# Performance work log

Measured on AMD Instinct MI355X. Metric: run time of the kernel, lower is better.

## Reference

```python
import jax, jax.numpy as jnp
import numpy as np

B, C, H, W = 16, 3, 128, 128
PATCH = 8
E = 512          # embedding_dim
NH = 8           # num_heads
P = 64           # proj_dim
HID = 2048       # hidden_dim
L = 6            # num_layers
COND = 3
PH, PW = H // PATCH, W // PATCH
S = PH * PW + 1  # sequence length (patches + cond token)
INV_SQRT_E = 1.0 / np.float32(np.sqrt(E))

_PARAM_SHAPES = {
    'patch_w': (E, C, PATCH, PATCH), 'patch_b': (E,),
    'cond_w1': (COND, E), 'cond_b1': (E,), 'cond_w2': (E, E), 'cond_b2': (E,),
    'pos_embed': (1, S, E),
    'enc_vp': (L, NH, E, P), 'enc_kp': (L, NH, E, P), 'enc_qh': (L, NH, S, S), 'enc_lift': (L, 1, NH * P, E),
    'enc_ln1g': (L, E), 'enc_ln1b': (L, E),
    'enc_w1': (L, E, HID), 'enc_b1': (L, HID), 'enc_w2': (L, HID, E), 'enc_b2': (L, E),
    'enc_ln2g': (L, E), 'enc_ln2b': (L, E),
    'dec_vp': (L, NH, E, P), 'dec_kp': (L, NH, E, P), 'dec_qh': (L, NH, S, S), 'dec_lift': (L, 1, NH * P, E),
    'dec_ln2g': (L, E), 'dec_ln2b': (L, E),
    'dec_w1': (L, E, HID), 'dec_b1': (L, HID), 'dec_w2': (L, HID, E), 'dec_b2': (L, E),
    'dec_ln3g': (L, E), 'dec_ln3b': (L, E),
    'final_g': (E,), 'final_b': (E,),
    'deconv_w': (E, C, PATCH, PATCH), 'deconv_b': (C,),
}


def setup_inputs() -> dict:
    key = jax.random.key(0)
    inp = {
        'x': jax.random.normal(jax.random.fold_in(key, 1000), (B, C, H, W), jnp.float32),
        'y': jax.random.normal(jax.random.fold_in(key, 1001), (B, COND), jnp.float32),
    }
    for i, (name, shp) in enumerate(_PARAM_SHAPES.items()):
        w = 0.02 * jax.random.normal(jax.random.fold_in(key, i), shp, jnp.float32)
        if name.endswith('g'):  # layernorm gains near 1
            w = w + 1.0
        inp[name] = w
    return inp


def _ln(x, g, b, eps=1e-5):
    m = x.mean(-1, keepdims=True)
    v = ((x - m) ** 2).mean(-1, keepdims=True)
    return (x - m) * jax.lax.rsqrt(v + eps) * g + b


def _mhsa(x, vp, kp, qh, lift):
    # x: (B,S,E); vp/kp: (NH,E,P); qh: (NH,S,S); lift: (1, NH*P, E)
    k = jnp.einsum('bse,hep->bhsp', x, kp)
    v = jnp.einsum('bse,hep->bhsp', x, vp)
    qv = jnp.einsum('hst,bhtp->bhsp', qh, v)
    # a_ts = (qh@V) @ K^T, then transpose(-2,-1): a[t,s] = qv[s] . k[t]
    a = jnp.einsum('bhsp,bhtp->bhts', qv, k) * INV_SQRT_E
    a = jax.nn.softmax(a, axis=-1)
    o = jnp.einsum('bhst,bhtp->bhsp', a, v)          # (B,NH,S,P)
    o = o.transpose(0, 2, 1, 3).reshape(x.shape[0], S, NH * P)
    return o @ lift[0]


def _block(z, vp, kp, qh, lift, g1, b1, w1, fb1, w2, fb2, g2, b2):
    z = _ln(z + _mhsa(z, vp, kp, qh, lift), g1, b1)
    h = jax.nn.leaky_relu(z @ w1 + fb1, 0.2) @ w2 + fb2  # dropout = identity (eval)
    return _ln(z + h, g2, b2)


def reference(x, y, patch_w, patch_b, cond_w1, cond_b1, cond_w2, cond_b2, pos_embed,
              enc_vp, enc_kp, enc_qh, enc_lift, enc_ln1g, enc_ln1b,
              enc_w1, enc_b1, enc_w2, enc_b2, enc_ln2g, enc_ln2b,
              dec_vp, dec_kp, dec_qh, dec_lift, dec_ln2g, dec_ln2b,
              dec_w1, dec_b1, dec_w2, dec_b2, dec_ln3g, dec_ln3b,
              final_g, final_b, deconv_w, deconv_b):
    b = x.shape[0]
    # Patching: Conv2d(k=p, s=p) == block-reshape + einsum
    xp = x.reshape(b, C, PH, PATCH, PW, PATCH)
    tok = jnp.einsum('bchpwq,ecpq->bhwe', xp, patch_w).reshape(b, PH * PW, E) + patch_b
    cond = jax.nn.leaky_relu(y @ cond_w1 + cond_b1, 0.2)
    cond = jax.nn.leaky_relu(cond @ cond_w2 + cond_b2, 0.2)
    z = jnp.concatenate([cond[:, None, :], tok], axis=1) + pos_embed
    for i in range(L):
        z = _block(z, enc_vp[i], enc_kp[i], enc_qh[i], enc_lift[i],
                   enc_ln1g[i], enc_ln1b[i], enc_w1[i], enc_b1[i],
                   enc_w2[i], enc_b2[i], enc_ln2g[i], enc_ln2b[i])
    for i in range(L):  # decoder: only mhsa_2 / ln2 / ff / ln3 are used
        z = _block(z, dec_vp[i], dec_kp[i], dec_qh[i], dec_lift[i],
                   dec_ln2g[i], dec_ln2b[i], dec_w1[i], dec_b1[i],
                   dec_w2[i], dec_b2[i], dec_ln3g[i], dec_ln3b[i])
    z = _ln(z[:, 1:], final_g, final_b)               # drop cond token
    g = z.reshape(b, PH, PW, E)                        # (B,E,PH,PW) grid, channels-last form
    out = jnp.einsum('bhwe,ecpq->bchpwq', g, deconv_w).reshape(b, C, H, W)
    return out + deconv_b[None, :, None, None]
```

## Files before the change

kernel.cpp:

```cpp
#include <hip/hip_runtime.h>
#include <stdint.h>
#include <math.h>

#define B_    16
#define C_    3
#define HIMG  128
#define E_    512
#define NH_   8
#define S_    257
#define T_    256
#define MTOK  4096
#define MSEQ  4112
#define HID_  2048
#define SP_   288
#define SLAB  (288*288)
#define PS    2105344L
#define INV_SQRT_E 0.044194173824159216f

typedef __attribute__((ext_vector_type(8))) __bf16 bf16x8;
typedef __attribute__((ext_vector_type(4))) float f32x4;

__device__ __forceinline__ void gload16(const void* g, const void* lds)
{
    __builtin_amdgcn_global_load_lds(
        (const __attribute__((address_space(1))) uint32_t*)(uintptr_t)g,
        (__attribute__((address_space(3))) uint32_t*)(uint32_t)(uintptr_t)lds,
        16, 0, 0);
}

template<int WMW, int WNW, bool LEAKY, bool OUTF32, bool VSPLIT>
__device__ __forceinline__ void gemm_core(
    const __bf16* __restrict__ A, int lda,
    const __bf16* __restrict__ Bt, int ldb,
    void* __restrict__ C, int ldc,
    const float* __restrict__ bias, float scale,
    int M, int N, int K, int tm, int tn, __bf16* __restrict__ vTout)
{
    constexpr int BM  = WMW * 64;
    constexpr int BN  = WNW * 32;
    constexpr int T   = WMW * WNW * 64;
    constexpr int ACH = BM * 4;
    constexpr int BCH = BN * 4;
    constexpr int LPT = ACH / T + BCH / T;
    __shared__ __align__(16) __bf16 sA[4][BM * 32];
    __shared__ __align__(16) __bf16 sB[4][BN * 32];

    const int tid  = threadIdx.x;
    const int lane = tid & 63;
    const int wid  = tid >> 6;
    const int wm   = wid / WNW;
    const int wn   = wid % WNW;
    const int lh   = lane >> 4;
    const int ll   = lane & 15;

    const __bf16* Ab = A + (long)tm * BM * lda;
    const __bf16* Bb = Bt + (long)tn * BN * ldb;

    f32x4 acc[4][2] = {};
    const int nst = K >> 5;

    auto stage = [&](int buf, int k0) {
#pragma unroll
        for (int rr = 0; rr < ACH / T; ++rr) {
            const int L = rr * T + tid;
            const int row = L >> 2;
            const int gch = (L & 3) ^ ((row >> 1) & 3);
            gload16(Ab + (long)row * lda + k0 + gch * 8,
                    (const char*)(&sA[buf][0]) + (rr * T + (wid << 6)) * 16);
        }
#pragma unroll
        for (int rr = 0; rr < BCH / T; ++rr) {
            const int L = rr * T + tid;
            const int row = L >> 2;
            const int gch = (L & 3) ^ ((row >> 1) & 3);
            gload16(Bb + (long)row * ldb + k0 + gch * 8,
                    (const char*)(&sB[buf][0]) + (rr * T + (wid << 6)) * 16);
        }
    };

    const int PF = nst < 3 ? nst : 3;
    for (int s = 0; s < PF; ++s) stage(s & 3, s << 5);

    for (int st = 0; st < nst; ++st) {
        const int rem = nst - 1 - st;
        if (rem >= 2)      asm volatile("s_waitcnt vmcnt(%0)" :: "n"(2 * LPT) : "memory");
        else if (rem == 1) asm volatile("s_waitcnt vmcnt(%0)" :: "n"(LPT) : "memory");
        else               asm volatile("s_waitcnt vmcnt(0)" ::: "memory");
        __builtin_amdgcn_s_barrier();
        __builtin_amdgcn_sched_barrier(0);

        if (st + 3 < nst) stage((st + 3) & 3, (st + 3) << 5);

        const int cur = st & 3;
        bf16x8 afr[4], bfr[2];
#pragma unroll
        for (int i = 0; i < 4; ++i) {
            const int rw = wm * 64 + i * 16 + ll;
            const int c  = lh ^ ((rw >> 1) & 3);
            afr[i] = *reinterpret_cast<const bf16x8*>(&sA[cur][rw * 32 + c * 8]);
        }
#pragma unroll
        for (int j = 0; j < 2; ++j) {
            const int rw = wn * 32 + j * 16 + ll;
            const int c  = lh ^ ((rw >> 1) & 3);
            bfr[j] = *reinterpret_cast<const bf16x8*>(&sB[cur][rw * 32 + c * 8]);
        }
#pragma unroll
        for (int i = 0; i < 4; ++i)
#pragma unroll
            for (int j = 0; j < 2; ++j)
                acc[i][j] = __builtin_amdgcn_mfma_f32_16x16x32_bf16(
                                afr[i], bfr[j], acc[i][j], 0, 0, 0);
    }

#pragma unroll
    for (int i = 0; i < 4; ++i)
#pragma unroll
        for (int ii = 0; ii < 4; ++ii) {
            const int m = tm * BM + wm * 64 + i * 16 + lh * 4 + ii;
            if (m >= M) continue;
#pragma unroll
            for (int j = 0; j < 2; ++j) {
                const int n = tn * BN + wn * 32 + j * 16 + ll;
                if (n >= N) continue;
                float v = acc[i][j][ii] * scale;
                if (bias) v += bias[n];
                if (LEAKY) v = v > 0.f ? v : 0.2f * v;
                if (VSPLIT && n >= 512) {
                    const int b = m / S_;
                    const int t = m - b * S_;
                    const int hp = n - 512;
                    vTout[(((long)(b * 8 + (hp >> 6)) * 64) + (hp & 63)) * SP_ + t] =
                        (__bf16)v;
                } else if (OUTF32) {
                    ((float*)C)[(long)m * ldc + n] = v;
                } else {
                    ((__bf16*)C)[(long)m * ldc + n] = (__bf16)v;
                }
            }
        }
}

__device__ __forceinline__ int xcd_swizzle(int wg, int nwg)
{
    const int q = nwg >> 3, r = nwg & 7;
    if (q == 0) return wg;
    const int xcd = wg & 7, off = wg >> 3;
    return (xcd < r ? xcd * (q + 1) : r * (q + 1) + (xcd - r) * q) + off;
}

template<int WMW, int WNW, bool LEAKY, bool OUTF32, bool VSPLIT>
__global__ __launch_bounds__(WMW * WNW * 64) void gemm_k(
    const __bf16* __restrict__ A, int lda, const __bf16* __restrict__ Bt, int ldb,
    void* __restrict__ C, int ldc, const float* __restrict__ bias, float scale,
    int M, int N, int K, int ntn, __bf16* __restrict__ vTout)
{
    const int wg = xcd_swizzle(blockIdx.x, gridDim.x);
    gemm_core<WMW, WNW, LEAKY, OUTF32, VSPLIT>(A, lda, Bt, ldb, C, ldc, bias, scale,
                                               M, N, K, wg / ntn, wg % ntn, vTout);
}

template<int WMW, int WNW>
__global__ __launch_bounds__(WMW * WNW * 64) void gemm_split_k(
    const __bf16* __restrict__ A, int lda, const __bf16* __restrict__ Bt, int ldb,
    __bf16* __restrict__ P, long pstride, const float* __restrict__ bias,
    int M, int N, int K, int npart, int ntn)
{
    const int part = blockIdx.y;
    const int Kp = K / npart;
    const int wg = xcd_swizzle(blockIdx.x, gridDim.x);
    gemm_core<WMW, WNW, false, false, false>(A + (long)part * Kp, lda,
                                             Bt + (long)part * Kp, ldb,
                                             P + (long)part * pstride, N,
                                             part == 0 ? bias : nullptr, 1.f,
                                             M, N, Kp, wg / ntn, wg % ntn, nullptr);
}

__global__ __launch_bounds__(256) void qv_k(const __bf16* __restrict__ qhb,
                                            const __bf16* __restrict__ vT,
                                            __bf16* __restrict__ qvcat)
{
    const int bh = blockIdx.z, b = bh >> 3, h = bh & 7;
    gemm_core<2, 2, false, false, false>(qhb + (long)h * SLAB, SP_,
                                         vT + (long)bh * 64 * SP_, SP_,
                                         qvcat + (long)b * S_ * E_ + h * 64, E_,
                                         nullptr, 1.f, S_, 64, SP_, blockIdx.x, 0,
                                         nullptr);
}

__global__ __launch_bounds__(256) void fa_k(const __bf16* __restrict__ kcat,
                                            const __bf16* __restrict__ qvcat,
                                            const __bf16* __restrict__ vT,
                                            __bf16* __restrict__ ocat)
{
    __shared__ __align__(16) __bf16 sK[64 * 64], sQV[64 * 64], sV[64 * 64];
    __shared__ __align__(16) __bf16 sP[4][16 * 64];
    const int bh = blockIdx.y, b = bh >> 3, h = bh & 7;
    const int i0 = blockIdx.x * 64;
    const int tid = threadIdx.x, lane = tid & 63, wid = tid >> 6;
    const int ll = lane & 15, lh = lane >> 4;

    const __bf16* kSrc = kcat + ((long)(b * S_ + i0)) * 512 + h * 64;
    const __bf16* qvB  = qvcat + (long)b * S_ * E_ + h * 64;
    const __bf16* vTb  = vT + (long)bh * 64 * SP_;

    auto stage64 = [&](__bf16* lds, const __bf16* src, int ldsrc) {
#pragma unroll
        for (int r = 0; r < 2; ++r) {
            const int L = r * 256 + wid * 64 + lane;
            const int row = L >> 3, c = L & 7;
            const int sc = c ^ (row & 7);
            gload16(src + (long)row * ldsrc + sc * 8,
                    (const char*)lds + (r * 256 + wid * 64) * 16);
        }
    };

    stage64(sK, kSrc, 512);
    stage64(sQV, qvB, E_);
    stage64(sV, vTb, SP_);
    __syncthreads();

    bf16x8 ka[2];
#pragma unroll
    for (int ks = 0; ks < 2; ++ks) {
        const int row = wid * 16 + ll;
        ka[ks] = *reinterpret_cast<const bf16x8*>(
            &sK[row * 64 + (((ks * 4 + lh) ^ (row & 7)) << 3)]);
    }

    float m[4], l[4];
#pragma unroll
    for (int ii = 0; ii < 4; ++ii) { m[ii] = -1e30f; l[ii] = 0.f; }
    f32x4 oacc[4] = {};

    for (int jt = 0; jt < 5; ++jt) {
        const int j0 = jt * 64;
        f32x4 s[4] = {};
#pragma unroll
        for (int ks = 0; ks < 2; ++ks)
#pragma unroll
            for (int nf = 0; nf < 4; ++nf) {
                const int row = nf * 16 + ll;
                const bf16x8 qb = *reinterpret_cast<const bf16x8*>(
                    &sQV[row * 64 + (((ks * 4 + lh) ^ (row & 7)) << 3)]);
                s[nf] = __builtin_amdgcn_mfma_f32_16x16x32_bf16(ka[ks], qb, s[nf], 0, 0, 0);
            }
        float pv[4][4];
#pragma unroll
        for (int ii = 0; ii < 4; ++ii) {
            float mx = -1e30f;
#pragma unroll
            for (int nf = 0; nf < 4; ++nf) {
                float sv = s[nf][ii] * INV_SQRT_E;
                if (j0 + nf * 16 + ll >= S_) sv = -1e30f;
                pv[nf][ii] = sv;
                mx = fmaxf(mx, sv);
            }
#pragma unroll
            for (int msk = 1; msk < 16; msk <<= 1) mx = fmaxf(mx, __shfl_xor(mx, msk));
            const float mnew = fmaxf(m[ii], mx);
            const float resc = __expf(m[ii] - mnew);
            m[ii] = mnew;
            float sum = 0.f;
#pragma unroll
            for (int nf = 0; nf < 4; ++nf) {
                const float e = __expf(pv[nf][ii] - mnew);
                pv[nf][ii] = e; sum += e;
            }
#pragma unroll
            for (int msk = 1; msk < 16; msk <<= 1) sum += __shfl_xor(sum, msk);
            l[ii] = l[ii] * resc + sum;
#pragma unroll
            for (int pf = 0; pf < 4; ++pf) oacc[pf][ii] *= resc;
        }
        __bf16* sPw = &sP[wid][0];
#pragma unroll
        for (int nf = 0; nf < 4; ++nf)
#pragma unroll
            for (int ii = 0; ii < 4; ++ii) {
                const int row = lh * 4 + ii, col = ll + 16 * nf;
                sPw[row * 64 + ((((col >> 3) ^ (row & 7)) << 3) | (col & 7))] =
                    (__bf16)pv[nf][ii];
            }
#pragma unroll
        for (int ks = 0; ks < 2; ++ks) {
            const bf16x8 pa = *reinterpret_cast<const bf16x8*>(
                &sPw[ll * 64 + (((ks * 4 + lh) ^ (ll & 7)) << 3)]);
#pragma unroll
            for (int pf = 0; pf < 4; ++pf) {
                const int row = pf * 16 + ll;
                const bf16x8 vb = *reinterpret_cast<const bf16x8*>(
                    &sV[row * 64 + (((ks * 4 + lh) ^ (row & 7)) << 3)]);
                oacc[pf] = __builtin_amdgcn_mfma_f32_16x16x32_bf16(pa, vb, oacc[pf], 0, 0, 0);
            }
        }
        if (jt < 4) {
            __syncthreads();
            stage64(sQV, qvB + (long)(j0 + 64) * E_, E_);
            stage64(sV, vTb + j0 + 64, SP_);
            __syncthreads();
        }
    }
#pragma unroll
    for (int ii = 0; ii < 4; ++ii) {
        const int i = i0 + wid * 16 + lh * 4 + ii;
        if (i >= S_) continue;
        const float invl = 1.f / l[ii];
#pragma unroll
        for (int pf = 0; pf < 4; ++pf)
            ocat[((long)(b * S_ + i)) * E_ + h * 64 + pf * 16 + ll] =
                (__bf16)(oacc[pf][ii] * invl);
    }
}

__global__ void ln_kernel(const __bf16* x,
                          const __bf16* __restrict__ parts, int nparts, long pstride,
                          const float* __restrict__ g, const float* __restrict__ bb,
                          __bf16* outb, int skip_cond, int nrows)
{
    const int row = blockIdx.x * 4 + (threadIdx.x >> 6);
    if (row >= nrows) return;
    const int lane = threadIdx.x & 63;
    const long xrow = skip_cond ? (long)row + (row >> 8) + 1 : (long)row;
    const bf16x8 xa = *reinterpret_cast<const bf16x8*>(x + xrow * E_ + lane * 8);
    float e[8];
#pragma unroll
    for (int i = 0; i < 8; ++i) e[i] = (float)xa[i];
    for (int p = 0; p < nparts; ++p) {
        const bf16x8 pv = *reinterpret_cast<const bf16x8*>(
            parts + (long)p * pstride + (long)row * E_ + lane * 8);
#pragma unroll
        for (int i = 0; i < 8; ++i) e[i] += (float)pv[i];
    }
    float s = 0.f;
#pragma unroll
    for (int i = 0; i < 8; ++i) s += e[i];
#pragma unroll
    for (int o = 32; o; o >>= 1) s += __shfl_xor(s, o);
    const float mean = s * (1.f / 512.f);
    float v = 0.f;
#pragma unroll
    for (int i = 0; i < 8; ++i) { e[i] -= mean; v += e[i] * e[i]; }
#pragma unroll
    for (int o = 32; o; o >>= 1) v += __shfl_xor(v, o);
    const float inv = rsqrtf(v * (1.f / 512.f) + 1e-5f);
    const float4* gp = (const float4*)g + lane * 2;
    const float4* bp = (const float4*)bb + lane * 2;
    const float4 g0 = gp[0], g1 = gp[1], bb0 = bp[0], bb1 = bp[1];
    const float gv[8] = {g0.x, g0.y, g0.z, g0.w, g1.x, g1.y, g1.z, g1.w};
    const float bv[8] = {bb0.x, bb0.y, bb0.z, bb0.w, bb1.x, bb1.y, bb1.z, bb1.w};
    bf16x8 ov;
#pragma unroll
    for (int i = 0; i < 8; ++i) ov[i] = (__bf16)(e[i] * inv * gv[i] + bv[i]);
    *reinterpret_cast<bf16x8*>(outb + (long)row * E_ + lane * 8) = ov;
}

__global__ void conv_straight(const float* __restrict__ in, __bf16* __restrict__ out, long n)
{
    const long i = (long)blockIdx.x * 256 + threadIdx.x;
    if (i < n) out[i] = (__bf16)in[i];
}

__global__ void conv_transpose(const float* __restrict__ in, __bf16* __restrict__ out,
                               int R, int C)
{
    __shared__ float tile[32][33];
    const int r0 = blockIdx.x * 32, c0 = blockIdx.y * 32;
    const int tx = threadIdx.x & 31, ty = threadIdx.x >> 5;
#pragma unroll
    for (int i = 0; i < 32; i += 8) {
        const int rr = r0 + ty + i, cc = c0 + tx;
        tile[ty + i][tx] = (rr < R && cc < C) ? in[(long)rr * C + cc] : 0.f;
    }
    __syncthreads();
#pragma unroll
    for (int i = 0; i < 32; i += 8) {
        const int cc = c0 + ty + i, rr = r0 + tx;
        if (cc < C && rr < R) out[(long)cc * R + rr] = (__bf16)tile[tx][ty + i];
    }
}

__global__ void wconv_all(const float* __restrict__ enc_kp, const float* __restrict__ dec_kp,
                          const float* __restrict__ enc_vp, const float* __restrict__ dec_vp,
                          const float* __restrict__ enc_lift, const float* __restrict__ dec_lift,
                          const float* __restrict__ enc_w1, const float* __restrict__ dec_w1,
                          const float* __restrict__ enc_w2, const float* __restrict__ dec_w2,
                          __bf16* __restrict__ kvT, __bf16* __restrict__ liftT,
                          __bf16* __restrict__ w1T, __bf16* __restrict__ w2T)
{
    const int lyr = blockIdx.z;
    const bool enc = lyr < 6;
    const int li = enc ? lyr : lyr - 6;
    const int j = blockIdx.y;
    const float* src; __bf16* dst; int R, C, nb;
    switch (j) {
        case 0:  src = (enc ? enc_kp : dec_kp) + (long)li * 262144;
                 dst = kvT + (long)lyr * 524288;            R = 512; C = 64;   nb = 8; break;
        case 1:  src = (enc ? enc_vp : dec_vp) + (long)li * 262144;
                 dst = kvT + (long)lyr * 524288 + 262144;   R = 512; C = 64;   nb = 8; break;
        case 2:  src = (enc ? enc_lift : dec_lift) + (long)li * 262144;
                 dst = liftT + (long)lyr * 262144;          R = 512; C = 512;  nb = 1; break;
        case 3:  src = (enc ? enc_w1 : dec_w1) + (long)li * 1048576;
                 dst = w1T + (long)lyr * 1048576;           R = 512; C = 2048; nb = 1; break;
        default: src = (enc ? enc_w2 : dec_w2) + (long)li * 1048576;
                 dst = w2T + (long)lyr * 1048576;           R = 2048; C = 512; nb = 1; break;
    }
    const int tR = R >> 5, tC = C >> 5;
    int t = blockIdx.x;
    if (t >= tR * tC * nb) return;
    const int bt = t / (tR * tC);
    t %= tR * tC;
    const int rt = t / tC, ct = t % tC;
    const long bs = (long)R * C;
    const float* ip = src + (long)bt * bs;
    __bf16* op = dst + (long)bt * bs;
    __shared__ float tile[32][33];
    const int tx = threadIdx.x & 31, ty = threadIdx.x >> 5;
#pragma unroll
    for (int i = 0; i < 32; i += 8)
        tile[ty + i][tx] = ip[(long)(rt * 32 + ty + i) * C + ct * 32 + tx];
    __syncthreads();
#pragma unroll
    for (int i = 0; i < 32; i += 8)
        op[(long)(ct * 32 + ty + i) * R + rt * 32 + tx] = (__bf16)tile[tx][ty + i];
}

__global__ void conv_qh_all(const float* __restrict__ enc_qh,
                            const float* __restrict__ dec_qh,
                            __bf16* __restrict__ out)
{
    const long n = 12L * 8 * SLAB;
    for (long o = (long)blockIdx.x * 256 + threadIdx.x; o < n; o += (long)gridDim.x * 256) {
        const int t = (int)(o % SP_);
        const long rr = o / SP_;
        const int s = (int)(rr % SP_);
        const long hh = rr / SP_;
        const int h = (int)(hh % 8);
        const int lyr = (int)(hh / 8);
        float v = 0.f;
        if (s < S_ && t < S_) {
            const float* src = (lyr < 6 ? enc_qh + (long)lyr * 8 * S_ * S_
                                        : dec_qh + (long)(lyr - 6) * 8 * S_ * S_);
            v = src[((long)h * S_ + s) * S_ + t];
        }
        out[o] = (__bf16)v;
    }
}

__global__ void vpad_kernel(__bf16* __restrict__ vT)
{
    const int i = blockIdx.x * 256 + threadIdx.x;
    if (i >= 128 * 64 * 31) return;
    const int t = 257 + (i % 31);
    const long rp = i / 31;
    vT[rp * SP_ + t] = (__bf16)0.f;
}

__global__ void im2col_kernel(const float* __restrict__ x, __bf16* __restrict__ xcol)
{
    const int idx = blockIdx.x * 256 + threadIdx.x;
    if (idx >= MTOK * 192) return;
    const int m = idx / 192, k = idx % 192;
    const int b = m >> 8, t = m & 255;
    const int ph = t >> 4, pw = t & 15;
    const int c = k >> 6, rr = k & 63;
    const int p = rr >> 3, q = rr & 7;
    xcol[idx] = (__bf16)x[(((long)(b * C_ + c) * HIMG) + ph * 8 + p) * HIMG + pw * 8 + q];
}

__global__ void cond_kernel(const float* __restrict__ y,
                            const float* __restrict__ w1, const float* __restrict__ b1,
                            const float* __restrict__ w2, const float* __restrict__ b2,
                            const float* __restrict__ pos, __bf16* __restrict__ zb)
{
    __shared__ float c1[512];
    const int b = blockIdx.x;
    const int e = threadIdx.x;
    float v = y[b * 3 + 0] * w1[e] + y[b * 3 + 1] * w1[512 + e]
            + y[b * 3 + 2] * w1[1024 + e] + b1[e];
    v = v > 0.f ? v : 0.2f * v;
    c1[e] = v;
    __syncthreads();
    float acc = b2[e];
    for (int k = 0; k < 512; ++k) acc += c1[k] * w2[k * 512 + e];
    acc = acc > 0.f ? acc : 0.2f * acc;
    zb[(long)b * S_ * E_ + e] = (__bf16)(acc + pos[e]);
}

__global__ void assemble_kernel(const __bf16* __restrict__ tok,
                                const float* __restrict__ pos,
                                __bf16* __restrict__ zb)
{
    const int idx = blockIdx.x * 256 + threadIdx.x;
    if (idx >= MTOK * E_) return;
    const int m = idx >> 9;
    const int e = idx & 511;
    const int b = m >> 8, t = m & 255;
    const float o = (float)tok[idx] + pos[(1 + t) * E_ + e];
    zb[((long)b * S_ + 1 + t) * E_ + e] = (__bf16)o;
}

__global__ void scatter_kernel(const float* __restrict__ dtmp,
                               const float* __restrict__ db,
                               float* __restrict__ out)
{
    const int idx = blockIdx.x * 256 + threadIdx.x;
    if (idx >= B_ * C_ * HIMG * HIMG) return;
    const int b  = idx / (C_ * HIMG * HIMG);
    const int rm = idx % (C_ * HIMG * HIMG);
    const int c  = rm / (HIMG * HIMG);
    const int hh = (rm % (HIMG * HIMG)) / HIMG;
    const int ww = rm % HIMG;
    const int ph = hh >> 3, p = hh & 7;
    const int pw = ww >> 3, q = ww & 7;
    out[idx] = dtmp[((long)(b * 256 + ph * 16 + pw)) * 192 + c * 64 + p * 8 + q] + db[c];
}

extern "C" void kernel_launch(void* const* d_in, const int* in_sizes, int n_in,
                              void* d_out, int out_size, void* d_ws, size_t ws_size,
                              hipStream_t stream)
{
    const float* x        = (const float*)d_in[0];
    const float* y        = (const float*)d_in[1];
    const float* patch_w  = (const float*)d_in[2];
    const float* patch_b  = (const float*)d_in[3];
    const float* cond_w1  = (const float*)d_in[4];
    const float* cond_b1  = (const float*)d_in[5];
    const float* cond_w2  = (const float*)d_in[6];
    const float* cond_b2  = (const float*)d_in[7];
    const float* pos      = (const float*)d_in[8];
    const float* enc_vp   = (const float*)d_in[9];
    const float* enc_kp   = (const float*)d_in[10];
    const float* enc_qh   = (const float*)d_in[11];
    const float* enc_lift = (const float*)d_in[12];
    const float* enc_ln1g = (const float*)d_in[13];
    const float* enc_ln1b = (const float*)d_in[14];
    const float* enc_w1   = (const float*)d_in[15];
    const float* enc_b1   = (const float*)d_in[16];
    const float* enc_w2   = (const float*)d_in[17];
    const float* enc_b2   = (const float*)d_in[18];
    const float* enc_ln2g = (const float*)d_in[19];
    const float* enc_ln2b = (const float*)d_in[20];
    const float* dec_vp   = (const float*)d_in[21];
    const float* dec_kp   = (const float*)d_in[22];
    const float* dec_qh   = (const float*)d_in[23];
    const float* dec_lift = (const float*)d_in[24];
    const float* dec_ln2g = (const float*)d_in[25];
    const float* dec_ln2b = (const float*)d_in[26];
    const float* dec_w1   = (const float*)d_in[27];
    const float* dec_b1   = (const float*)d_in[28];
    const float* dec_w2   = (const float*)d_in[29];
    const float* dec_b2   = (const float*)d_in[30];
    const float* dec_ln3g = (const float*)d_in[31];
    const float* dec_ln3b = (const float*)d_in[32];
    const float* final_g  = (const float*)d_in[33];
    const float* final_b  = (const float*)d_in[34];
    const float* deconv_w = (const float*)d_in[35];
    const float* deconv_b = (const float*)d_in[36];
    float* out = (float*)d_out;

    char* wp = (char*)d_ws;
    auto alloc_f32 = [&](long n) { float* p = (float*)wp; wp += ((n * 4 + 63) & ~63LL); return p; };
    auto alloc_bf  = [&](long n) { __bf16* p = (__bf16*)wp; wp += ((n * 2 + 63) & ~63LL); return p; };

    float*  dtmp   = alloc_f32(786432);
    __bf16* zb     = alloc_bf(4352L * 512);
    __bf16* tok    = alloc_bf(4096L * 512);
    __bf16* xcolb  = alloc_bf(786432);
    __bf16* kcat   = alloc_bf(4352L * 512);
    __bf16* qvcat  = alloc_bf(4352L * 512);
    __bf16* ocat   = alloc_bf(4352L * 512);
    __bf16* vT     = alloc_bf(128L * 64 * SP_);
    __bf16* psl    = alloc_bf(4L * PS);
    __bf16* hidden = alloc_bf(4224L * 2048);
    __bf16* gbuf   = alloc_bf(4096L * 512);
    __bf16* pwb    = alloc_bf(512L * 192);
    __bf16* dwTb   = alloc_bf(192L * 512);
    __bf16* kvT12  = alloc_bf(12L * 524288);
    __bf16* liftT12= alloc_bf(12L * 262144);
    __bf16* w1T12  = alloc_bf(12L * 1048576);
    __bf16* w2T12  = alloc_bf(12L * 1048576);
    __bf16* qhb12  = alloc_bf(12L * 8 * SLAB + 96L * SP_);
    (void)ws_size; (void)in_sizes; (void)n_in; (void)out_size;

    const dim3 blk(256);

    conv_straight<<<dim3(384), blk, 0, stream>>>(patch_w, pwb, 98304);
    conv_transpose<<<dim3(16, 6), blk, 0, stream>>>(deconv_w, dwTb, 512, 192);
    wconv_all<<<dim3(1024, 5, 12), blk, 0, stream>>>(
        enc_kp, dec_kp, enc_vp, dec_vp, enc_lift, dec_lift,
        enc_w1, dec_w1, enc_w2, dec_w2, kvT12, liftT12, w1T12, w2T12);
    conv_qh_all<<<dim3(4096), blk, 0, stream>>>(enc_qh, dec_qh, qhb12);
    vpad_kernel<<<dim3(992), blk, 0, stream>>>(vT);

    im2col_kernel<<<dim3(3072), blk, 0, stream>>>(x, xcolb);
    gemm_k<2, 2, false, false, false><<<dim3(256), blk, 0, stream>>>(
        xcolb, 192, pwb, 192, tok, 512, patch_b, 1.f, MTOK, 512, 192, 8, nullptr);
    cond_kernel<<<dim3(B_), dim3(512), 0, stream>>>(y, cond_w1, cond_b1,
                                                    cond_w2, cond_b2, pos, zb);
    assemble_kernel<<<dim3(8192), blk, 0, stream>>>(tok, pos, zb);

    for (int l = 0; l < 12; ++l) {
        const bool enc = l < 6;
        const int  li  = enc ? l : l - 6;
        const float* g1   = (enc ? enc_ln1g : dec_ln2g) + li * E_;
        const float* bb1  = (enc ? enc_ln1b : dec_ln2b) + li * E_;
        const float* fb1  = (enc ? enc_b1   : dec_b1)   + li * HID_;
        const float* fb2  = (enc ? enc_b2   : dec_b2)   + li * E_;
        const float* g2   = (enc ? enc_ln2g : dec_ln3g) + li * E_;
        const float* bb2  = (enc ? enc_ln2b : dec_ln3b) + li * E_;
        const __bf16* kvTb   = kvT12 + (long)l * 524288;
        const __bf16* liftTb = liftT12 + (long)l * 262144;
        const __bf16* w1Tb   = w1T12 + (long)l * 1048576;
        const __bf16* w2Tb   = w2T12 + (long)l * 1048576;
        const __bf16* qhb    = qhb12 + (long)l * 8 * SLAB;

        gemm_k<2, 2, false, false, true><<<dim3(528), blk, 0, stream>>>(
            zb, 512, kvTb, 512, kcat, 512, nullptr, 1.f, MSEQ, 1024, 512, 16, vT);
        qv_k<<<dim3(3, 1, 128), blk, 0, stream>>>(qhb, vT, qvcat);
        fa_k<<<dim3(5, 128), blk, 0, stream>>>(kcat, qvcat, vT, ocat);
        gemm_split_k<2, 2><<<dim3(264, 2), blk, 0, stream>>>(
            ocat, 512, liftTb, 512, psl, PS, nullptr, MSEQ, 512, 512, 2, 8);
        ln_kernel<<<dim3(1028), blk, 0, stream>>>(zb, psl, 2, PS, g1, bb1,
                                                  zb, 0, MSEQ);

        gemm_k<2, 2, true, false, false><<<dim3(1056), blk, 0, stream>>>(
            zb, 512, w1Tb, 512, hidden, 2048, fb1, 1.f, MSEQ, HID_, 512, 32, nullptr);
        gemm_split_k<2, 2><<<dim3(264, 4), blk, 0, stream>>>(
            hidden, 2048, w2Tb, 2048, psl, PS, fb2, MSEQ, 512, HID_, 4, 8);
        ln_kernel<<<dim3(1028), blk, 0, stream>>>(zb, psl, 4, PS, g2, bb2,
                                                  zb, 0, MSEQ);
    }

    ln_kernel<<<dim3(1024), blk, 0, stream>>>(zb, nullptr, 0, 0, final_g, final_b,
                                              gbuf, 1, MTOK);
    gemm_k<2, 2, false, true, false><<<dim3(96), blk, 0, stream>>>(
        gbuf, 512, dwTb, 512, dtmp, 192, nullptr, 1.f, MTOK, 192, 512, 3, nullptr);
    scatter_kernel<<<dim3(3072), blk, 0, stream>>>(dtmp, deconv_b, out);
}
```

Baseline: 1.527 ms.

## Widen GEMM tiles to 128x128, use 3-stage pipeline, vectorize weight transpose

The GEMM core now uses 128xNF*32 tiles with NF=4 for most projections, giving 128x128 blocks with 4x4 MFMA per wave. This raises operand reuse per LDS load and halves the block count. The LDS ring drops from 4 to 3 buffers with a prefetch distance of 2, to fit the larger B tile in LDS. The lift projection moves from split-K 2 to split-K 4 to keep the grid filled. The weight-conversion transpose uses 64x64 tiles with 16-byte vectorized bf16 stores. The risks are less latency hiding from the shallower pipeline, and lower occupancy or wave-count tail effects on the smaller grids.

```diff
diff --git a/kernel.cpp b/kernel.cpp
--- a/kernel.cpp
+++ b/kernel.cpp
@@ -28,7 +28,7 @@
         16, 0, 0);
 }
 
-template<int WMW, int WNW, bool LEAKY, bool OUTF32, bool VSPLIT>
+template<int NF, bool LEAKY, bool OUTF32, bool VSPLIT>
 __device__ __forceinline__ void gemm_core(
     const __bf16* __restrict__ A, int lda,
     const __bf16* __restrict__ Bt, int ldb,
@@ -36,63 +36,63 @@
     const float* __restrict__ bias, float scale,
     int M, int N, int K, int tm, int tn, __bf16* __restrict__ vTout)
 {
-    constexpr int BM  = WMW * 64;
-    constexpr int BN  = WNW * 32;
-    constexpr int T   = WMW * WNW * 64;
+    constexpr int BM  = 128;
+    constexpr int BN  = NF * 32;
     constexpr int ACH = BM * 4;
     constexpr int BCH = BN * 4;
-    constexpr int LPT = ACH / T + BCH / T;
-    __shared__ __align__(16) __bf16 sA[4][BM * 32];
-    __shared__ __align__(16) __bf16 sB[4][BN * 32];
+    constexpr int LPT = ACH / 256 + BCH / 256;
+    __shared__ __align__(16) __bf16 sA[3][BM * 32];
+    __shared__ __align__(16) __bf16 sB[3][BN * 32];
 
     const int tid  = threadIdx.x;
     const int lane = tid & 63;
     const int wid  = tid >> 6;
-    const int wm   = wid / WNW;
-    const int wn   = wid % WNW;
+    const int wm   = wid >> 1;
+    const int wn   = wid & 1;
     const int lh   = lane >> 4;
     const int ll   = lane & 15;
 
     const __bf16* Ab = A + (long)tm * BM * lda;
     const __bf16* Bb = Bt + (long)tn * BN * ldb;
 
-    f32x4 acc[4][2] = {};
+    f32x4 acc[4][NF] = {};
     const int nst = K >> 5;
 
     auto stage = [&](int buf, int k0) {
 #pragma unroll
-        for (int rr = 0; rr < ACH / T; ++rr) {
-            const int L = rr * T + tid;
+        for (int rr = 0; rr < ACH / 256; ++rr) {
+            const int L = rr * 256 + tid;
             const int row = L >> 2;
             const int gch = (L & 3) ^ ((row >> 1) & 3);
             gload16(Ab + (long)row * lda + k0 + gch * 8,
-                    (const char*)(&sA[buf][0]) + (rr * T + (wid << 6)) * 16);
-        }
-#pragma unroll
-        for (int rr = 0; rr < BCH / T; ++rr) {
-            const int L = rr * T + tid;
+                    (const char*)(&sA[buf][0]) + (rr * 256 + (wid << 6)) * 16);
+        }
+#pragma unroll
+        for (int rr = 0; rr < BCH / 256; ++rr) {
+            const int L = rr * 256 + tid;
             const int row = L >> 2;
             const int gch = (L & 3) ^ ((row >> 1) & 3);
             gload16(Bb + (long)row * ldb + k0 + gch * 8,
-                    (const char*)(&sB[buf][0]) + (rr * T + (wid << 6)) * 16);
+                    (const char*)(&sB[buf][0]) + (rr * 256 + (wid << 6)) * 16);
         }
     };
 
-    const int PF = nst < 3 ? nst : 3;
-    for (int s = 0; s < PF; ++s) stage(s & 3, s << 5);
-
+    stage(0, 0);
+    if (nst > 1) stage(1, 32);
+
+    int cur = 0, pre = 2;
     for (int st = 0; st < nst; ++st) {
-        const int rem = nst - 1 - st;
-        if (rem >= 2)      asm volatile("s_waitcnt vmcnt(%0)" :: "n"(2 * LPT) : "memory");
-        else if (rem == 1) asm volatile("s_waitcnt vmcnt(%0)" :: "n"(LPT) : "memory");
-        else               asm volatile("s_waitcnt vmcnt(0)" ::: "memory");
+        if (st + 1 < nst) asm volatile("s_waitcnt vmcnt(%0)" :: "n"(LPT) : "memory");
+        else              asm volatile("s_waitcnt vmcnt(0)" ::: "memory");
         __builtin_amdgcn_s_barrier();
         __builtin_amdgcn_sched_barrier(0);
 
-        if (st + 3 < nst) stage((st + 3) & 3, (st + 3) << 5);
-
-        const int cur = st & 3;
-        bf16x8 afr[4], bfr[2];
+        if (st + 2 < nst) {
+            stage(pre, (st + 2) << 5);
+            pre = (pre == 2) ? 0 : pre + 1;
+        }
+
+        bf16x8 afr[4], bfr[NF];
 #pragma unroll
         for (int i = 0; i < 4; ++i) {
             const int rw = wm * 64 + i * 16 + ll;
@@ -100,17 +100,18 @@
             afr[i] = *reinterpret_cast<const bf16x8*>(&sA[cur][rw * 32 + c * 8]);
         }
 #pragma unroll
-        for (int j = 0; j < 2; ++j) {
-            const int rw = wn * 32 + j * 16 + ll;
+        for (int j = 0; j < NF; ++j) {
+            const int rw = wn * (NF * 16) + j * 16 + ll;
             const int c  = lh ^ ((rw >> 1) & 3);
             bfr[j] = *reinterpret_cast<const bf16x8*>(&sB[cur][rw * 32 + c * 8]);
         }
 #pragma unroll
         for (int i = 0; i < 4; ++i)
 #pragma unroll
-            for (int j = 0; j < 2; ++j)
+            for (int j = 0; j < NF; ++j)
                 acc[i][j] = __builtin_amdgcn_mfma_f32_16x16x32_bf16(
                                 afr[i], bfr[j], acc[i][j], 0, 0, 0);
+        cur = (cur == 2) ? 0 : cur + 1;
     }
 
 #pragma unroll
@@ -120,8 +121,8 @@
             const int m = tm * BM + wm * 64 + i * 16 + lh * 4 + ii;
             if (m >= M) continue;
 #pragma unroll
-            for (int j = 0; j < 2; ++j) {
-                const int n = tn * BN + wn * 32 + j * 16 + ll;
+            for (int j = 0; j < NF; ++j) {
+                const int n = tn * BN + wn * (NF * 16) + j * 16 + ll;
                 if (n >= N) continue;
                 float v = acc[i][j][ii] * scale;
                 if (bias) v += bias[n];
@@ -149,19 +150,18 @@
     return (xcd < r ? xcd * (q + 1) : r * (q + 1) + (xcd - r) * q) + off;
 }
 
-template<int WMW, int WNW, bool LEAKY, bool OUTF32, bool VSPLIT>
-__global__ __launch_bounds__(WMW * WNW * 64) void gemm_k(
+template<int NF, bool LEAKY, bool OUTF32, bool VSPLIT>
+__global__ __launch_bounds__(256) void gemm_k(
     const __bf16* __restrict__ A, int lda, const __bf16* __restrict__ Bt, int ldb,
     void* __restrict__ C, int ldc, const float* __restrict__ bias, float scale,
     int M, int N, int K, int ntn, __bf16* __restrict__ vTout)
 {
     const int wg = xcd_swizzle(blockIdx.x, gridDim.x);
-    gemm_core<WMW, WNW, LEAKY, OUTF32, VSPLIT>(A, lda, Bt, ldb, C, ldc, bias, scale,
-                                               M, N, K, wg / ntn, wg % ntn, vTout);
-}
-
-template<int WMW, int WNW>
-__global__ __launch_bounds__(WMW * WNW * 64) void gemm_split_k(
+    gemm_core<NF, LEAKY, OUTF32, VSPLIT>(A, lda, Bt, ldb, C, ldc, bias, scale,
+                                         M, N, K, wg / ntn, wg % ntn, vTout);
+}
+
+__global__ __launch_bounds__(256) void gemm_split_k(
     const __bf16* __restrict__ A, int lda, const __bf16* __restrict__ Bt, int ldb,
     __bf16* __restrict__ P, long pstride, const float* __restrict__ bias,
     int M, int N, int K, int npart, int ntn)
@@ -169,11 +169,11 @@
     const int part = blockIdx.y;
     const int Kp = K / npart;
     const int wg = xcd_swizzle(blockIdx.x, gridDim.x);
-    gemm_core<WMW, WNW, false, false, false>(A + (long)part * Kp, lda,
-                                             Bt + (long)part * Kp, ldb,
-                                             P + (long)part * pstride, N,
-                                             part == 0 ? bias : nullptr, 1.f,
-                                             M, N, Kp, wg / ntn, wg % ntn, nullptr);
+    gemm_core<4, false, false, false>(A + (long)part * Kp, lda,
+                                      Bt + (long)part * Kp, ldb,
+                                      P + (long)part * pstride, N,
+                                      part == 0 ? bias : nullptr, 1.f,
+                                      M, N, Kp, wg / ntn, wg % ntn, nullptr);
 }
 
 __global__ __launch_bounds__(256) void qv_k(const __bf16* __restrict__ qhb,
@@ -181,11 +181,11 @@
                                             __bf16* __restrict__ qvcat)
 {
     const int bh = blockIdx.z, b = bh >> 3, h = bh & 7;
-    gemm_core<2, 2, false, false, false>(qhb + (long)h * SLAB, SP_,
-                                         vT + (long)bh * 64 * SP_, SP_,
-                                         qvcat + (long)b * S_ * E_ + h * 64, E_,
-                                         nullptr, 1.f, S_, 64, SP_, blockIdx.x, 0,
-                                         nullptr);
+    gemm_core<2, false, false, false>(qhb + (long)h * SLAB, SP_,
+                                      vT + (long)bh * 64 * SP_, SP_,
+                                      qvcat + (long)b * S_ * E_ + h * 64, E_,
+                                      nullptr, 1.f, S_, 64, SP_, blockIdx.x, 0,
+                                      nullptr);
 }
 
 __global__ __launch_bounds__(256) void fa_k(const __bf16* __restrict__ kcat,
@@ -405,7 +405,7 @@
         default: src = (enc ? enc_w2 : dec_w2) + (long)li * 1048576;
                  dst = w2T + (long)lyr * 1048576;           R = 2048; C = 512; nb = 1; break;
     }
-    const int tR = R >> 5, tC = C >> 5;
+    const int tR = R >> 6, tC = C >> 6;
     int t = blockIdx.x;
     if (t >= tR * tC * nb) return;
     const int bt = t / (tR * tC);
@@ -414,15 +414,22 @@
     const long bs = (long)R * C;
     const float* ip = src + (long)bt * bs;
     __bf16* op = dst + (long)bt * bs;
-    __shared__ float tile[32][33];
-    const int tx = threadIdx.x & 31, ty = threadIdx.x >> 5;
-#pragma unroll
-    for (int i = 0; i < 32; i += 8)
-        tile[ty + i][tx] = ip[(long)(rt * 32 + ty + i) * C + ct * 32 + tx];
+    __shared__ float tile[64][65];
+    const int tx = threadIdx.x & 63, ty = threadIdx.x >> 6;
+#pragma unroll
+    for (int i = 0; i < 64; i += 4)
+        tile[ty + i][tx] = ip[(long)(rt * 64 + ty + i) * C + ct * 64 + tx];
     __syncthreads();
-#pragma unroll
-    for (int i = 0; i < 32; i += 8)
-        op[(long)(ct * 32 + ty + i) * R + rt * 32 + tx] = (__bf16)tile[tx][ty + i];
+    const int cw = threadIdx.x >> 3;
+    const int r0 = (threadIdx.x & 7) * 8;
+#pragma unroll
+    for (int pass = 0; pass < 2; ++pass) {
+        const int c = pass * 32 + cw;
+        bf16x8 v;
+#pragma unroll
+        for (int k = 0; k < 8; ++k) v[k] = (__bf16)tile[r0 + k][c];
+        *reinterpret_cast<bf16x8*>(&op[(long)(ct * 64 + c) * R + rt * 64 + r0]) = v;
+    }
 }
 
 __global__ void conv_qh_all(const float* __restrict__ enc_qh,
@@ -587,15 +594,15 @@
 
     conv_straight<<<dim3(384), blk, 0, stream>>>(patch_w, pwb, 98304);
     conv_transpose<<<dim3(16, 6), blk, 0, stream>>>(deconv_w, dwTb, 512, 192);
-    wconv_all<<<dim3(1024, 5, 12), blk, 0, stream>>>(
+    wconv_all<<<dim3(256, 5, 12), blk, 0, stream>>>(
         enc_kp, dec_kp, enc_vp, dec_vp, enc_lift, dec_lift,
         enc_w1, dec_w1, enc_w2, dec_w2, kvT12, liftT12, w1T12, w2T12);
     conv_qh_all<<<dim3(4096), blk, 0, stream>>>(enc_qh, dec_qh, qhb12);
     vpad_kernel<<<dim3(992), blk, 0, stream>>>(vT);
 
     im2col_kernel<<<dim3(3072), blk, 0, stream>>>(x, xcolb);
-    gemm_k<2, 2, false, false, false><<<dim3(256), blk, 0, stream>>>(
-        xcolb, 192, pwb, 192, tok, 512, patch_b, 1.f, MTOK, 512, 192, 8, nullptr);
+    gemm_k<4, false, false, false><<<dim3(128), blk, 0, stream>>>(
+        xcolb, 192, pwb, 192, tok, 512, patch_b, 1.f, MTOK, 512, 192, 4, nullptr);
     cond_kernel<<<dim3(B_), dim3(512), 0, stream>>>(y, cond_w1, cond_b1,
                                                     cond_w2, cond_b2, pos, zb);
     assemble_kernel<<<dim3(8192), blk, 0, stream>>>(tok, pos, zb);
@@ -615,26 +622,26 @@
         const __bf16* w2Tb   = w2T12 + (long)l * 1048576;
         const __bf16* qhb    = qhb12 + (long)l * 8 * SLAB;
 
-        gemm_k<2, 2, false, false, true><<<dim3(528), blk, 0, stream>>>(
-            zb, 512, kvTb, 512, kcat, 512, nullptr, 1.f, MSEQ, 1024, 512, 16, vT);
+        gemm_k<4, false, false, true><<<dim3(264), blk, 0, stream>>>(
+            zb, 512, kvTb, 512, kcat, 512, nullptr, 1.f, MSEQ, 1024, 512, 8, vT);
         qv_k<<<dim3(3, 1, 128), blk, 0, stream>>>(qhb, vT, qvcat);
         fa_k<<<dim3(5, 128), blk, 0, stream>>>(kcat, qvcat, vT, ocat);
-        gemm_split_k<2, 2><<<dim3(264, 2), blk, 0, stream>>>(
-            ocat, 512, liftTb, 512, psl, PS, nullptr, MSEQ, 512, 512, 2, 8);
-        ln_kernel<<<dim3(1028), blk, 0, stream>>>(zb, psl, 2, PS, g1, bb1,
+        gemm_split_k<<<dim3(132, 4), blk, 0, stream>>>(
+            ocat, 512, liftTb, 512, psl, PS, nullptr, MSEQ, 512, 512, 4, 4);
+        ln_kernel<<<dim3(1028), blk, 0, stream>>>(zb, psl, 4, PS, g1, bb1,
                                                   zb, 0, MSEQ);
 
-        gemm_k<2, 2, true, false, false><<<dim3(1056), blk, 0, stream>>>(
-            zb, 512, w1Tb, 512, hidden, 2048, fb1, 1.f, MSEQ, HID_, 512, 32, nullptr);
-        gemm_split_k<2, 2><<<dim3(264, 4), blk, 0, stream>>>(
-            hidden, 2048, w2Tb, 2048, psl, PS, fb2, MSEQ, 512, HID_, 4, 8);
+        gemm_k<4, true, false, false><<<dim3(528), blk, 0, stream>>>(
+            zb, 512, w1Tb, 512, hidden, 2048, fb1, 1.f, MSEQ, HID_, 512, 16, nullptr);
+        gemm_split_k<<<dim3(132, 4), blk, 0, stream>>>(
+            hidden, 2048, w2Tb, 2048, psl, PS, fb2, MSEQ, 512, HID_, 4, 4);
         ln_kernel<<<dim3(1028), blk, 0, stream>>>(zb, psl, 4, PS, g2, bb2,
                                                   zb, 0, MSEQ);
     }
 
     ln_kernel<<<dim3(1024), blk, 0, stream>>>(zb, nullptr, 0, 0, final_g, final_b,
                                               gbuf, 1, MTOK);
-    gemm_k<2, 2, false, true, false><<<dim3(96), blk, 0, stream>>>(
-        gbuf, 512, dwTb, 512, dtmp, 192, nullptr, 1.f, MTOK, 192, 512, 3, nullptr);
+    gemm_k<4, false, true, false><<<dim3(64), blk, 0, stream>>>(
+        gbuf, 512, dwTb, 512, dtmp, 192, nullptr, 1.f, MTOK, 192, 512, 2, nullptr);
     scatter_kernel<<<dim3(3072), blk, 0, stream>>>(dtmp, deconv_b, out);
 }
```

After: 1.584 ms. 3.7% more time.
